# Performance work log

Hardware: AMD Instinct MI355X
Metric: run time of the kernel (lower is better)

## Reference

```python
import jax, jax.numpy as jnp
import numpy as np

N, F_IN, H = 8192, 128, 256
AVG_DEG_P = 16.0 / N  # ~16 neighbors per node, BA-graph-like sparsity


def setup_inputs() -> dict:
    key = jax.random.key(0)
    ks = jax.random.split(key, 16)
    # symmetric 0/1 adjacency, no self-loops
    B = jax.random.bernoulli(ks[0], AVG_DEG_P, (N, N)).astype(jnp.float32)
    A = jnp.maximum(B, B.T)
    A = A * (1.0 - jnp.eye(N, dtype=jnp.float32))
    features = jax.random.normal(ks[1], (N, F_IN), dtype=jnp.float32)
    treatments = jax.random.bernoulli(ks[2], 0.1, (N, 1)).astype(jnp.float32)
    def glorot(k, shape):
        lim = float(np.sqrt(6.0 / (shape[0] + shape[1])))
        return jax.random.uniform(k, shape, jnp.float32, -lim, lim)
    return {
        "A": A,
        "features": features,
        "treatments": treatments,
        "W1": glorot(ks[3], (F_IN, H)),   # GCNConv layer 1 weight
        "b1": jnp.zeros((H,), jnp.float32),
        "W2": glorot(ks[4], (H, H)),      # GCNConv layer 2 weight
        "b2": jnp.zeros((H,), jnp.float32),
        "W_emb": glorot(ks[5], (H + 1, H)),
        "b_emb": jnp.zeros((H,), jnp.float32),
        "W_t0": glorot(ks[6], (H, 1)),
        "b_t0": jnp.zeros((1,), jnp.float32),
        "W_t1": glorot(ks[7], (H, 1)),
        "b_t1": jnp.zeros((1,), jnp.float32),
    }


def _gcn_norm(A):
    # PyG GCNConv default: D^-1/2 (A + I) D^-1/2
    A_hat = A + jnp.eye(A.shape[0], dtype=A.dtype)
    d = jnp.sum(A_hat, axis=1)
    dinv = jnp.where(d > 0, 1.0 / jnp.sqrt(d), 0.0)
    return A_hat * dinv[:, None] * dinv[None, :]


def reference(A, features, treatments, W1, b1, W2, b2, W_emb, b_emb, W_t0, b_t0, W_t1, b_t1):
    nA = _gcn_norm(A)                                  # [N, N]
    h = jax.nn.relu(nA @ (features @ W1) + b1)         # GCNConv 1, [N, H]
    h = jax.nn.relu(nA @ (h @ W2) + b2)                # GCNConv 2, [N, H]
    deg = jnp.sum(A, axis=1) + 1e-8                    # [N]
    # faithful to torch: (A * treatments).sum(dim=1) broadcasts treatments[N,1] over columns
    exposure = (jnp.sum(A * treatments, axis=1) / deg)[:, None]  # [N, 1]
    rep = jnp.concatenate([h, exposure], axis=1)       # [N, H+1]
    emb = jax.nn.relu(rep @ W_emb + b_emb)             # [N, H]
    y0_pred = (emb @ W_t0 + b_t0).reshape(-1)          # [N]
    y1_pred = (emb @ W_t1 + b_t1).reshape(-1)          # [N]
    return (y0_pred, y1_pred, emb)
```

## Files before the change

kernel.cpp:

```cpp
#include <hip/hip_runtime.h>

#define NN   8192
#define FIN  128
#define HH   256
#define CAP  128

typedef float    f32x4 __attribute__((ext_vector_type(4)));
typedef float    f32x2 __attribute__((ext_vector_type(2)));
typedef _Float16 f16x4 __attribute__((ext_vector_type(4)));
typedef _Float16 f16x2 __attribute__((ext_vector_type(2)));

__device__ __forceinline__ const f32x4* c4(const float* p) { return (const f32x4*)p; }
__device__ __forceinline__       f32x4* p4(float* p)       { return (f32x4*)p; }
__device__ __forceinline__ const f32x2* c2(const float* p) { return (const f32x2*)p; }
__device__ __forceinline__       f32x2* p2(float* p)       { return (f32x2*)p; }

__global__ __launch_bounds__(256) void k_build(
    const float* __restrict__ A, const float* __restrict__ treat,
    const float* __restrict__ X,
    int* __restrict__ cols, int* __restrict__ cnt,
    float* __restrict__ dinv, float* __restrict__ expo,
    _Float16* __restrict__ Xh)
{
  const int row = blockIdx.x;
  if (row >= NN) {
    const int t0 = (row - NN) * 256 + threadIdx.x;
    for (int i = t0; i < NN * FIN / 4; i += 128 * 256) {
      const f32x4 v = *c4(&X[(size_t)i * 4]);
      f16x4 h = {(_Float16)v[0], (_Float16)v[1], (_Float16)v[2], (_Float16)v[3]};
      *(f16x4*)&Xh[(size_t)i * 4] = h;
    }
    return;
  }

  const f32x4* Ar = c4(A + (size_t)row * NN);
  __shared__ int   s_cnt;
  __shared__ float s_rs[4];
  if (threadIdx.x == 0) s_cnt = 0;
  __syncthreads();

  float rs = 0.f;
  int* myCols = cols + (size_t)row * CAP;
  #pragma unroll
  for (int it = 0; it < NN / 4 / 256; ++it) {
    const int idx = it * 256 + threadIdx.x;
    const f32x4 a = __builtin_nontemporal_load(Ar + idx);
    const int base = idx * 4;
    #pragma unroll
    for (int u = 0; u < 4; ++u) {
      if (a[u] != 0.0f) {
        rs += a[u];
        int p = atomicAdd(&s_cnt, 1);
        if (p < CAP) myCols[p] = base + u;
      }
    }
  }
  #pragma unroll
  for (int off = 32; off > 0; off >>= 1) rs += __shfl_down(rs, off);
  const int wid = threadIdx.x >> 6;
  if ((threadIdx.x & 63) == 0) s_rs[wid] = rs;
  __syncthreads();
  if (threadIdx.x == 0) {
    const float R = s_rs[0] + s_rs[1] + s_rs[2] + s_rs[3];
    int n = s_cnt; if (n > CAP) n = CAP;
    cnt[row]  = n;
    dinv[row] = rsqrtf(R + 1.0f);
    expo[row] = treat[row] * R / (R + 1e-8f);
  }
}

__global__ __launch_bounds__(256) void k_agg0h(
    const _Float16* __restrict__ Xh,
    const int* __restrict__ cols, const int* __restrict__ cnt,
    const float* __restrict__ dinv, float* __restrict__ out)
{
  const int wid  = threadIdx.x >> 6;
  const int lane = threadIdx.x & 63;
  const int i    = blockIdx.x * 4 + wid;
  __shared__ int   s_cols[4][CAP];
  __shared__ float s_w[4][CAP];

  const int n = cnt[i];
  if (lane < n) {
    const int j = cols[(size_t)i * CAP + lane];
    s_cols[wid][lane] = j;  s_w[wid][lane] = dinv[j];
  }
  if (lane + 64 < n) {
    const int j = cols[(size_t)i * CAP + lane + 64];
    s_cols[wid][lane + 64] = j;  s_w[wid][lane + 64] = dinv[j];
  }
  __syncthreads();

  const float di = dinv[i];
  const f16x2 sv = *(const f16x2*)&Xh[(size_t)i * FIN + 2 * lane];
  f32x2 acc = {di * (float)sv[0], di * (float)sv[1]};
  #pragma unroll 4
  for (int t = 0; t < n; ++t) {
    const int   j = s_cols[wid][t];
    const float w = s_w[wid][t];
    const f16x2 v = *(const f16x2*)&Xh[(size_t)j * FIN + 2 * lane];
    acc[0] += w * (float)v[0];
    acc[1] += w * (float)v[1];
  }
  *p2(&out[(size_t)i * FIN + 2 * lane]) = di * acc;
}

template<bool INIT>
__global__ __launch_bounds__(256) void k_aggh(
    const _Float16* __restrict__ M,
    const int* __restrict__ cols, const int* __restrict__ cnt,
    const float* __restrict__ dinv, const float* __restrict__ bias,
    float* __restrict__ out,
    float* __restrict__ dout, const float* __restrict__ bt0, const float* __restrict__ bt1)
{
  const int wid  = threadIdx.x >> 6;
  const int lane = threadIdx.x & 63;
  const int i    = blockIdx.x * 4 + wid;
  __shared__ int   s_cols[4][CAP];
  __shared__ float s_w[4][CAP];

  if constexpr (INIT) {
    if (blockIdx.x < 64) {
      const int idx = blockIdx.x * 256 + threadIdx.x;
      dout[idx] = (idx < NN) ? bt0[0] : bt1[0];
    }
  }

  const int n = cnt[i];
  if (lane < n) {
    const int j = cols[(size_t)i * CAP + lane];
    s_cols[wid][lane] = j;  s_w[wid][lane] = dinv[j];
  }
  if (lane + 64 < n) {
    const int j = cols[(size_t)i * CAP + lane + 64];
    s_cols[wid][lane + 64] = j;  s_w[wid][lane + 64] = dinv[j];
  }
  __syncthreads();

  const float di = dinv[i];
  const f32x4 bias4 = *c4(&bias[lane * 4]);
  const f16x4 sv = *(const f16x4*)&M[(size_t)i * HH + 4 * lane];
  f32x4 acc = {di * (float)sv[0], di * (float)sv[1],
               di * (float)sv[2], di * (float)sv[3]};
  #pragma unroll 4
  for (int t = 0; t < n; ++t) {
    const int   j = s_cols[wid][t];
    const float w = s_w[wid][t];
    const f16x4 v = *(const f16x4*)&M[(size_t)j * HH + 4 * lane];
    acc[0] += w * (float)v[0];
    acc[1] += w * (float)v[1];
    acc[2] += w * (float)v[2];
    acc[3] += w * (float)v[3];
  }
  f32x4 o = di * acc + bias4;
  #pragma unroll
  for (int q = 0; q < 4; ++q) o[q] = fmaxf(o[q], 0.f);
  *p4(&out[(size_t)i * HH + 4 * lane]) = o;
}

template<int K, bool RELU, bool EXPO, bool HEADS, bool F16OUT>
__device__ __forceinline__ void gemm_body(
    int bidx,
    const float* __restrict__ M, const float* __restrict__ W,
    const float* __restrict__ bias, const float* __restrict__ expo,
    const float* __restrict__ Wt0, const float* __restrict__ Wt1,
    float* __restrict__ out, _Float16* __restrict__ out16,
    float* __restrict__ y0, float* __restrict__ y1,
    float (*As)[64], float (*Bs)[64])
{
  const int tid = threadIdx.x;
  const int tx = tid & 15, ty = tid >> 4;
  const int bx = bidx & 127, by = bidx >> 7;
  const int r0 = bx * 64, c0 = by * 64;
  const int la_r = tid & 63;
  const int la_k = (tid >> 6) << 2;
  const int lb_k = tid >> 4;
  const int lb_c = (tid & 15) << 2;

  const float* Abase = M + (size_t)(r0 + la_r) * K + la_k;
  const float* Bbase = W + (size_t)lb_k * HH + c0 + lb_c;

  f32x4 aR = *c4(Abase);
  f32x4 bR = *c4(Bbase);
  float acc[4][4] = {};

  #pragma unroll 1
  for (int k0 = 0; k0 < K; k0 += 16) {
    As[la_k + 0][la_r] = aR[0];
    As[la_k + 1][la_r] = aR[1];
    As[la_k + 2][la_r] = aR[2];
    As[la_k + 3][la_r] = aR[3];
    *p4(&Bs[lb_k][lb_c]) = bR;
    __syncthreads();
    if (k0 + 16 < K) {
      aR = *c4(Abase + k0 + 16);
      bR = *c4(Bbase + (size_t)(k0 + 16) * HH);
    }
    #pragma unroll
    for (int kk = 0; kk < 16; ++kk) {
      const f32x4 av = *c4(&As[kk][ty * 4]);
      const f32x4 bv = *c4(&Bs[kk][tx * 4]);
      #pragma unroll
      for (int i = 0; i < 4; ++i)
        #pragma unroll
        for (int j = 0; j < 4; ++j)
          acc[i][j] += av[i] * bv[j];
    }
    __syncthreads();
  }

  f32x4 eb = {0.f, 0.f, 0.f, 0.f}, bs = {0.f, 0.f, 0.f, 0.f};
  if constexpr (RELU) bs = *c4(&bias[c0 + tx * 4]);
  if constexpr (EXPO) eb = *c4(&W[(size_t)K * HH + c0 + tx * 4]);
  f32x4 wt0 = {0.f, 0.f, 0.f, 0.f}, wt1 = {0.f, 0.f, 0.f, 0.f};
  if constexpr (HEADS) {
    wt0 = *c4(&Wt0[c0 + tx * 4]);
    wt1 = *c4(&Wt1[c0 + tx * 4]);
  }
  #pragma unroll
  for (int i = 0; i < 4; ++i) {
    const int r = r0 + ty * 4 + i;
    f32x4 o;
    if constexpr (RELU) {
      float e = 0.f;
      if constexpr (EXPO) e = expo[r];
      #pragma unroll
      for (int j = 0; j < 4; ++j) {
        float v = acc[i][j] + bs[j];
        if constexpr (EXPO) v += e * eb[j];
        o[j] = fmaxf(v, 0.f);
      }
    } else {
      #pragma unroll
      for (int j = 0; j < 4; ++j) o[j] = acc[i][j];
    }
    if constexpr (F16OUT) {
      f16x4 oh = {(_Float16)o[0], (_Float16)o[1], (_Float16)o[2], (_Float16)o[3]};
      *(f16x4*)&out16[(size_t)r * HH + c0 + tx * 4] = oh;
    } else {
      *p4(&out[(size_t)r * HH + c0 + tx * 4]) = o;
    }
    if constexpr (HEADS) {
      float s0 = o[0] * wt0[0] + o[1] * wt0[1] + o[2] * wt0[2] + o[3] * wt0[3];
      float s1 = o[0] * wt1[0] + o[1] * wt1[1] + o[2] * wt1[2] + o[3] * wt1[3];
      #pragma unroll
      for (int off = 8; off > 0; off >>= 1) {
        s0 += __shfl_down(s0, off);
        s1 += __shfl_down(s1, off);
      }
      if ((tid & 15) == 0) {
        atomicAdd(&y0[r], s0);
        atomicAdd(&y1[r], s1);
      }
    }
  }
}

template<int K, bool RELU, bool EXPO, bool HEADS, bool F16OUT>
__global__ __launch_bounds__(256) void k_gemm(
    const float* __restrict__ M, const float* __restrict__ W,
    const float* __restrict__ bias, const float* __restrict__ expo,
    const float* __restrict__ Wt0, const float* __restrict__ Wt1,
    float* __restrict__ out, _Float16* __restrict__ out16,
    float* __restrict__ y0, float* __restrict__ y1)
{
  __shared__ float As[16][64];
  __shared__ float Bs[16][64];
  gemm_body<K, RELU, EXPO, HEADS, F16OUT>(blockIdx.x, M, W, bias, expo, Wt0, Wt1,
                                          out, out16, y0, y1, As, Bs);
}

extern "C" void kernel_launch(void* const* d_in, const int* in_sizes, int n_in,
                              void* d_out, int out_size, void* d_ws, size_t ws_size,
                              hipStream_t stream)
{
  const float* A      = (const float*)d_in[0];
  const float* feats  = (const float*)d_in[1];
  const float* treat  = (const float*)d_in[2];
  const float* W1     = (const float*)d_in[3];
  const float* b1     = (const float*)d_in[4];
  const float* W2     = (const float*)d_in[5];
  const float* b2     = (const float*)d_in[6];
  const float* W_emb  = (const float*)d_in[7];
  const float* b_emb  = (const float*)d_in[8];
  const float* W_t0   = (const float*)d_in[9];
  const float* b_t0   = (const float*)d_in[10];
  const float* W_t1   = (const float*)d_in[11];
  const float* b_t1   = (const float*)d_in[12];
  float* dout = (float*)d_out;

  int*      cols   = (int*)d_ws;
  int*      cnt    = cols + (size_t)NN * CAP;
  float*    dinv   = (float*)(cnt + NN);
  float*    expo   = dinv + NN;
  float*    bufX   = expo + NN;
  float*    bufB   = bufX + (size_t)NN * FIN;
  _Float16* Xh     = (_Float16*)(bufB + (size_t)NN * HH);
  _Float16* bufA16 = Xh + (size_t)NN * FIN;

  float* y0  = dout;
  float* y1  = dout + NN;
  float* emb = dout + 2 * NN;

  k_build<<<NN + 128, 256, 0, stream>>>(A, treat, feats, cols, cnt, dinv, expo, Xh);
  k_agg0h<<<NN / 4, 256, 0, stream>>>(Xh, cols, cnt, dinv, bufX);
  k_gemm<FIN, true, false, false, false><<<512, 256, 0, stream>>>(
      bufX, W1, b1, nullptr, nullptr, nullptr, bufB, nullptr, nullptr, nullptr);
  k_gemm<HH, false, false, false, true><<<512, 256, 0, stream>>>(
      bufB, W2, nullptr, nullptr, nullptr, nullptr, nullptr, bufA16, nullptr, nullptr);
  k_aggh<true><<<NN / 4, 256, 0, stream>>>(bufA16, cols, cnt, dinv, b2, bufB,
                                           dout, b_t0, b_t1);
  k_gemm<HH, true, true, true, false><<<512, 256, 0, stream>>>(
      bufB, W_emb, b_emb, expo, W_t0, W_t1, emb, nullptr, y0, y1);
}
```

Before: 430.9 us.

## Use fp16 MFMA for the two 256-wide GEMMs with pre-transposed fp16 weights

Measured after the change: 433.9 us. Within noise of the previous version (+0.7%).

```diff
diff --git a/kernel.cpp b/kernel.cpp
--- a/kernel.cpp
+++ b/kernel.cpp
@@ -7,6 +7,7 @@
 
 typedef float    f32x4 __attribute__((ext_vector_type(4)));
 typedef float    f32x2 __attribute__((ext_vector_type(2)));
+typedef _Float16 f16x8 __attribute__((ext_vector_type(8)));
 typedef _Float16 f16x4 __attribute__((ext_vector_type(4)));
 typedef _Float16 f16x2 __attribute__((ext_vector_type(2)));
 
@@ -18,17 +19,32 @@
 __global__ __launch_bounds__(256) void k_build(
     const float* __restrict__ A, const float* __restrict__ treat,
     const float* __restrict__ X,
+    const float* __restrict__ W2, const float* __restrict__ W_emb,
     int* __restrict__ cols, int* __restrict__ cnt,
     float* __restrict__ dinv, float* __restrict__ expo,
-    _Float16* __restrict__ Xh)
+    _Float16* __restrict__ Xh, _Float16* __restrict__ W2T,
+    _Float16* __restrict__ WembT)
 {
   const int row = blockIdx.x;
   if (row >= NN) {
-    const int t0 = (row - NN) * 256 + threadIdx.x;
-    for (int i = t0; i < NN * FIN / 4; i += 128 * 256) {
-      const f32x4 v = *c4(&X[(size_t)i * 4]);
-      f16x4 h = {(_Float16)v[0], (_Float16)v[1], (_Float16)v[2], (_Float16)v[3]};
-      *(f16x4*)&Xh[(size_t)i * 4] = h;
+    const int q = row - NN;
+    if (q < 128) {
+      const int t0 = q * 256 + threadIdx.x;
+      for (int i = t0; i < NN * FIN / 4; i += 128 * 256) {
+        const f32x4 v = *c4(&X[(size_t)i * 4]);
+        f16x4 h = {(_Float16)v[0], (_Float16)v[1], (_Float16)v[2], (_Float16)v[3]};
+        *(f16x4*)&Xh[(size_t)i * 4] = h;
+      }
+    } else if (q < 132) {
+      for (int e = (q - 128) * 256 + threadIdx.x; e < HH * HH; e += 1024) {
+        const int k = e >> 8, n = e & 255;
+        W2T[(size_t)n * HH + k] = (_Float16)W2[e];
+      }
+    } else {
+      for (int e = (q - 132) * 256 + threadIdx.x; e < HH * HH; e += 1024) {
+        const int k = e >> 8, n = e & 255;
+        WembT[(size_t)n * HH + k] = (_Float16)W_emb[e];
+      }
     }
     return;
   }
@@ -110,7 +126,7 @@
     const _Float16* __restrict__ M,
     const int* __restrict__ cols, const int* __restrict__ cnt,
     const float* __restrict__ dinv, const float* __restrict__ bias,
-    float* __restrict__ out,
+    _Float16* __restrict__ out,
     float* __restrict__ dout, const float* __restrict__ bt0, const float* __restrict__ bt1)
 {
   const int wid  = threadIdx.x >> 6;
@@ -153,24 +169,95 @@
     acc[3] += w * (float)v[3];
   }
   f32x4 o = di * acc + bias4;
-  #pragma unroll
-  for (int q = 0; q < 4; ++q) o[q] = fmaxf(o[q], 0.f);
-  *p4(&out[(size_t)i * HH + 4 * lane]) = o;
-}
-
-template<int K, bool RELU, bool EXPO, bool HEADS, bool F16OUT>
-__device__ __forceinline__ void gemm_body(
-    int bidx,
-    const float* __restrict__ M, const float* __restrict__ W,
+  f16x4 oh;
+  #pragma unroll
+  for (int q = 0; q < 4; ++q) oh[q] = (_Float16)fmaxf(o[q], 0.f);
+  *(f16x4*)&out[(size_t)i * HH + 4 * lane] = oh;
+}
+
+template<bool FIN_EPI>
+__global__ __launch_bounds__(256) void k_gemm_mfma(
+    const _Float16* __restrict__ Ah, const _Float16* __restrict__ BT,
+    const float* __restrict__ Wfull,
     const float* __restrict__ bias, const float* __restrict__ expo,
     const float* __restrict__ Wt0, const float* __restrict__ Wt1,
     float* __restrict__ out, _Float16* __restrict__ out16,
-    float* __restrict__ y0, float* __restrict__ y1,
-    float (*As)[64], float (*Bs)[64])
-{
+    float* __restrict__ y0, float* __restrict__ y1)
+{
+  const int tid = threadIdx.x;
+  const int w = tid >> 6, l = tid & 63;
+  const int r0 = (blockIdx.x & 127) * 64 + w * 16;
+  const int c0 = (blockIdx.x >> 7) * 64;
+  const int lr = l & 15;
+  const int lk = (l >> 4) * 8;
+
+  f32x4 acc[4] = {{0.f,0.f,0.f,0.f},{0.f,0.f,0.f,0.f},
+                  {0.f,0.f,0.f,0.f},{0.f,0.f,0.f,0.f}};
+  const _Float16* Aptr = Ah + (size_t)(r0 + lr) * HH + lk;
+  const _Float16* Bptr = BT + (size_t)(c0 + lr) * HH + lk;
+
+  #pragma unroll
+  for (int k0 = 0; k0 < HH; k0 += 32) {
+    const f16x8 a = *(const f16x8*)(Aptr + k0);
+    #pragma unroll
+    for (int nt = 0; nt < 4; ++nt) {
+      const f16x8 b = *(const f16x8*)(Bptr + (size_t)nt * 16 * HH + k0);
+      acc[nt] = __builtin_amdgcn_mfma_f32_16x16x32_f16(a, b, acc[nt], 0, 0, 0);
+    }
+  }
+
+  const int rbase = r0 + (l >> 4) * 4;
+  if constexpr (!FIN_EPI) {
+    #pragma unroll
+    for (int r = 0; r < 4; ++r)
+      #pragma unroll
+      for (int nt = 0; nt < 4; ++nt)
+        out16[(size_t)(rbase + r) * HH + c0 + 16 * nt + lr] = (_Float16)acc[nt][r];
+  } else {
+    float eb[4], bs[4], w0[4], w1[4];
+    #pragma unroll
+    for (int nt = 0; nt < 4; ++nt) {
+      const int c = c0 + 16 * nt + lr;
+      eb[nt] = Wfull[(size_t)HH * HH + c];
+      bs[nt] = bias[c];
+      w0[nt] = Wt0[c];
+      w1[nt] = Wt1[c];
+    }
+    #pragma unroll
+    for (int r = 0; r < 4; ++r) {
+      const int R = rbase + r;
+      const float e = expo[R];
+      float s0 = 0.f, s1 = 0.f;
+      #pragma unroll
+      for (int nt = 0; nt < 4; ++nt) {
+        float v = fmaxf(acc[nt][r] + e * eb[nt] + bs[nt], 0.f);
+        out[(size_t)R * HH + c0 + 16 * nt + lr] = v;
+        s0 += v * w0[nt];
+        s1 += v * w1[nt];
+      }
+      #pragma unroll
+      for (int off = 8; off > 0; off >>= 1) {
+        s0 += __shfl_down(s0, off);
+        s1 += __shfl_down(s1, off);
+      }
+      if (lr == 0) {
+        atomicAdd(&y0[R], s0);
+        atomicAdd(&y1[R], s1);
+      }
+    }
+  }
+}
+
+template<int K>
+__global__ __launch_bounds__(256) void k_gemm_v(
+    const float* __restrict__ M, const float* __restrict__ W,
+    const float* __restrict__ bias, _Float16* __restrict__ out16)
+{
+  __shared__ float As[16][64];
+  __shared__ float Bs[16][64];
   const int tid = threadIdx.x;
   const int tx = tid & 15, ty = tid >> 4;
-  const int bx = bidx & 127, by = bidx >> 7;
+  const int bx = blockIdx.x & 127, by = blockIdx.x >> 7;
   const int r0 = bx * 64, c0 = by * 64;
   const int la_r = tid & 63;
   const int la_k = (tid >> 6) << 2;
@@ -209,65 +296,15 @@
     __syncthreads();
   }
 
-  f32x4 eb = {0.f, 0.f, 0.f, 0.f}, bs = {0.f, 0.f, 0.f, 0.f};
-  if constexpr (RELU) bs = *c4(&bias[c0 + tx * 4]);
-  if constexpr (EXPO) eb = *c4(&W[(size_t)K * HH + c0 + tx * 4]);
-  f32x4 wt0 = {0.f, 0.f, 0.f, 0.f}, wt1 = {0.f, 0.f, 0.f, 0.f};
-  if constexpr (HEADS) {
-    wt0 = *c4(&Wt0[c0 + tx * 4]);
-    wt1 = *c4(&Wt1[c0 + tx * 4]);
-  }
+  const f32x4 bs = *c4(&bias[c0 + tx * 4]);
   #pragma unroll
   for (int i = 0; i < 4; ++i) {
     const int r = r0 + ty * 4 + i;
-    f32x4 o;
-    if constexpr (RELU) {
-      float e = 0.f;
-      if constexpr (EXPO) e = expo[r];
-      #pragma unroll
-      for (int j = 0; j < 4; ++j) {
-        float v = acc[i][j] + bs[j];
-        if constexpr (EXPO) v += e * eb[j];
-        o[j] = fmaxf(v, 0.f);
-      }
-    } else {
-      #pragma unroll
-      for (int j = 0; j < 4; ++j) o[j] = acc[i][j];
-    }
-    if constexpr (F16OUT) {
-      f16x4 oh = {(_Float16)o[0], (_Float16)o[1], (_Float16)o[2], (_Float16)o[3]};
-      *(f16x4*)&out16[(size_t)r * HH + c0 + tx * 4] = oh;
-    } else {
-      *p4(&out[(size_t)r * HH + c0 + tx * 4]) = o;
-    }
-    if constexpr (HEADS) {
-      float s0 = o[0] * wt0[0] + o[1] * wt0[1] + o[2] * wt0[2] + o[3] * wt0[3];
-      float s1 = o[0] * wt1[0] + o[1] * wt1[1] + o[2] * wt1[2] + o[3] * wt1[3];
-      #pragma unroll
-      for (int off = 8; off > 0; off >>= 1) {
-        s0 += __shfl_down(s0, off);
-        s1 += __shfl_down(s1, off);
-      }
-      if ((tid & 15) == 0) {
-        atomicAdd(&y0[r], s0);
-        atomicAdd(&y1[r], s1);
-      }
-    }
-  }
-}
-
-template<int K, bool RELU, bool EXPO, bool HEADS, bool F16OUT>
-__global__ __launch_bounds__(256) void k_gemm(
-    const float* __restrict__ M, const float* __restrict__ W,
-    const float* __restrict__ bias, const float* __restrict__ expo,
-    const float* __restrict__ Wt0, const float* __restrict__ Wt1,
-    float* __restrict__ out, _Float16* __restrict__ out16,
-    float* __restrict__ y0, float* __restrict__ y1)
-{
-  __shared__ float As[16][64];
-  __shared__ float Bs[16][64];
-  gemm_body<K, RELU, EXPO, HEADS, F16OUT>(blockIdx.x, M, W, bias, expo, Wt0, Wt1,
-                                          out, out16, y0, y1, As, Bs);
+    f16x4 oh;
+    #pragma unroll
+    for (int j = 0; j < 4; ++j) oh[j] = (_Float16)fmaxf(acc[i][j] + bs[j], 0.f);
+    *(f16x4*)&out16[(size_t)r * HH + c0 + tx * 4] = oh;
+  }
 }
 
 extern "C" void kernel_launch(void* const* d_in, const int* in_sizes, int n_in,
@@ -289,27 +326,32 @@
   const float* b_t1   = (const float*)d_in[12];
   float* dout = (float*)d_out;
 
-  int*      cols   = (int*)d_ws;
-  int*      cnt    = cols + (size_t)NN * CAP;
-  float*    dinv   = (float*)(cnt + NN);
-  float*    expo   = dinv + NN;
-  float*    bufX   = expo + NN;
-  float*    bufB   = bufX + (size_t)NN * FIN;
-  _Float16* Xh     = (_Float16*)(bufB + (size_t)NN * HH);
-  _Float16* bufA16 = Xh + (size_t)NN * FIN;
+  int*      cols  = (int*)d_ws;
+  int*      cnt   = cols + (size_t)NN * CAP;
+  float*    dinv  = (float*)(cnt + NN);
+  float*    expo  = dinv + NN;
+  float*    bufX  = expo + NN;
+  _Float16* Xh    = (_Float16*)(bufX + (size_t)NN * FIN);
+  _Float16* h1h   = Xh + (size_t)NN * FIN;
+  _Float16* h1w2h = h1h + (size_t)NN * HH;
+  _Float16* h2h   = h1w2h + (size_t)NN * HH;
+  _Float16* W2T   = h2h + (size_t)NN * HH;
+  _Float16* WembT = W2T + (size_t)HH * HH;
 
   float* y0  = dout;
   float* y1  = dout + NN;
   float* emb = dout + 2 * NN;
 
-  k_build<<<NN + 128, 256, 0, stream>>>(A, treat, feats, cols, cnt, dinv, expo, Xh);
+  k_build<<<NN + 136, 256, 0, stream>>>(A, treat, feats, W2, W_emb,
+                                        cols, cnt, dinv, expo, Xh, W2T, WembT);
   k_agg0h<<<NN / 4, 256, 0, stream>>>(Xh, cols, cnt, dinv, bufX);
-  k_gemm<FIN, true, false, false, false><<<512, 256, 0, stream>>>(
-      bufX, W1, b1, nullptr, nullptr, nullptr, bufB, nullptr, nullptr, nullptr);
-  k_gemm<HH, false, false, false, true><<<512, 256, 0, stream>>>(
-      bufB, W2, nullptr, nullptr, nullptr, nullptr, nullptr, bufA16, nullptr, nullptr);
-  k_aggh<true><<<NN / 4, 256, 0, stream>>>(bufA16, cols, cnt, dinv, b2, bufB,
+  k_gemm_v<FIN><<<512, 256, 0, stream>>>(bufX, W1, b1, h1h);
+  k_gemm_mfma<false><<<512, 256, 0, stream>>>(
+      h1h, W2T, nullptr, nullptr, nullptr, nullptr, nullptr,
+      nullptr, h1w2h, nullptr, nullptr);
+  k_aggh<true><<<NN / 4, 256, 0, stream>>>(h1w2h, cols, cnt, dinv, b2, h2h,
                                            dout, b_t0, b_t1);
-  k_gemm<HH, true, true, true, false><<<512, 256, 0, stream>>>(
-      bufB, W_emb, b_emb, expo, W_t0, W_t1, emb, nullptr, y0, y1);
-}
+  k_gemm_mfma<true><<<512, 256, 0, stream>>>(
+      h2h, WembT, W_emb, b_emb, expo, W_t0, W_t1,
+      emb, nullptr, y0, y1);
+}
```
